# Performance work log

Hardware: AMD Instinct MI355X
Metric: run time of the kernel (lower is better)

Reference implementation:

```python
import jax, jax.numpy as jnp
import numpy as np

B, D, H = 524288, 64, 19  # batch, input_size, hidden_size


def setup_inputs() -> dict:
    key = jax.random.key(0)
    ks = jax.random.split(key, 4)
    x = jax.random.normal(ks[0], (B, D), dtype=jnp.float32)
    # nn.Linear params (stored as [out, in] like torch)
    Wi = jax.random.normal(ks[1], (H, D), dtype=jnp.float32) / np.sqrt(D).astype(np.float32)
    bi = jnp.zeros((H,), jnp.float32)
    Wr = jax.random.normal(ks[2], (H, H), dtype=jnp.float32) / np.sqrt(H).astype(np.float32)
    Wo = jax.random.normal(ks[3], (H, H), dtype=jnp.float32) / np.sqrt(H).astype(np.float32)
    bo = jnp.zeros((H,), jnp.float32)
    tau = jnp.full((H,), 0.5, jnp.float32)        # nn.Parameter(ones*0.5)
    tau_adapt = jnp.full((H,), 0.1, jnp.float32)  # nn.Parameter(ones*0.1)
    return {"x": x, "Wi": Wi, "bi": bi, "Wr": Wr, "Wo": Wo, "bo": bo,
            "tau": tau, "tau_adapt": tau_adapt, "steps": 10}


def reference(x, Wi, bi, Wr, Wo, bo, tau, tau_adapt, steps):
    dt = 0.01
    # scalar urgency over the whole input, clamped from below
    urgency = jnp.maximum(jnp.abs(x).mean(), 0.01)
    tau_dyn = jnp.clip(tau * (1.0 - tau_adapt) + tau_adapt / urgency, 0.01, 10.0)  # [H]
    mapped = x @ Wi.T + bi  # [B, H], computed once outside the loop
    h0 = jnp.zeros((x.shape[0], tau.shape[0]), x.dtype)

    def step(h, _):
        act = jnp.tanh(mapped + h @ Wr.T)
        h = h + dt * ((-h + act) / tau_dyn)
        return h, None

    h, _ = jax.lax.scan(step, h0, None, length=steps)
    return (h @ Wo.T + bo, h)
```

## Files before the change

kernel.cpp:

```cpp
#include <hip/hip_runtime.h>

#define NB 524288
#define ND 64
#define NH 19

__device__ __forceinline__ float fast_tanh(float x) {
    x = fminf(9.0f, fmaxf(-9.0f, x));
    float e = __expf(2.0f * x);
    return 1.0f - 2.0f * __builtin_amdgcn_rcpf(e + 1.0f);
}

extern "C" __global__ void __launch_bounds__(256)
ltc_mapped_urgency(const float* __restrict__ x, const float* __restrict__ Wi,
                   const float* __restrict__ bi, float* __restrict__ mapped,
                   double* __restrict__ acc, int storeMapped)
{
    const int b = blockIdx.x * 256 + threadIdx.x;
    const float4* xr = (const float4*)(x + (size_t)b * ND);
    float m[NH];
#pragma unroll
    for (int j = 0; j < NH; ++j) m[j] = bi[j];
    float s = 0.f;
#pragma unroll
    for (int q = 0; q < ND / 4; ++q) {
        const float4 v = xr[q];
        s += fabsf(v.x) + fabsf(v.y) + fabsf(v.z) + fabsf(v.w);
#pragma unroll
        for (int j = 0; j < NH; ++j) {
            m[j] = fmaf(v.x, Wi[j * ND + 4 * q + 0], m[j]);
            m[j] = fmaf(v.y, Wi[j * ND + 4 * q + 1], m[j]);
            m[j] = fmaf(v.z, Wi[j * ND + 4 * q + 2], m[j]);
            m[j] = fmaf(v.w, Wi[j * ND + 4 * q + 3], m[j]);
        }
    }
    if (storeMapped) {
#pragma unroll
        for (int j = 0; j < NH; ++j) mapped[(size_t)j * NB + b] = m[j];
    }
#pragma unroll
    for (int off = 32; off > 0; off >>= 1) s += __shfl_down(s, off, 64);
    __shared__ float red[4];
    const int lane = threadIdx.x & 63, w = threadIdx.x >> 6;
    if (lane == 0) red[w] = s;
    __syncthreads();
    if (threadIdx.x == 0) atomicAdd(acc, (double)(red[0] + red[1] + red[2] + red[3]));
}

template <bool RECOMP, int ROWS>
__global__ void __launch_bounds__(256)
ltc_steps(const float* __restrict__ x, const float* __restrict__ Wi,
          const float* __restrict__ bi, const float* __restrict__ mapped,
          const double* __restrict__ acc,
          const float* __restrict__ Wr, const float* __restrict__ Wo,
          const float* __restrict__ bo, const float* __restrict__ tau,
          const float* __restrict__ ta, const int* __restrict__ steps_p,
          float* __restrict__ out)
{
    const int gid = blockIdx.x * 256 + threadIdx.x;
    const int T = NB / ROWS;
    const double mean = *acc * (1.0 / ((double)NB * (double)ND));
    const float u = fmaxf((float)mean, 0.01f);
    float rr_[NH];
#pragma unroll
    for (int j = 0; j < NH; ++j) {
        float t = tau[j] * (1.f - ta[j]) + ta[j] / u;
        t = fminf(10.f, fmaxf(0.01f, t));
        rr_[j] = 0.01f / t;
    }
    float m[ROWS][NH], h[ROWS][NH];
#pragma unroll
    for (int rI = 0; rI < ROWS; ++rI) {
        const int b = gid + rI * T;
        if (RECOMP) {
            const float4* xr = (const float4*)(x + (size_t)b * ND);
#pragma unroll
            for (int j = 0; j < NH; ++j) m[rI][j] = bi[j];
#pragma unroll
            for (int q = 0; q < ND / 4; ++q) {
                const float4 v = xr[q];
#pragma unroll
                for (int j = 0; j < NH; ++j) {
                    m[rI][j] = fmaf(v.x, Wi[j * ND + 4 * q + 0], m[rI][j]);
                    m[rI][j] = fmaf(v.y, Wi[j * ND + 4 * q + 1], m[rI][j]);
                    m[rI][j] = fmaf(v.z, Wi[j * ND + 4 * q + 2], m[rI][j]);
                    m[rI][j] = fmaf(v.w, Wi[j * ND + 4 * q + 3], m[rI][j]);
                }
            }
        } else {
#pragma unroll
            for (int j = 0; j < NH; ++j) m[rI][j] = mapped[(size_t)j * NB + b];
        }
#pragma unroll
        for (int j = 0; j < NH; ++j) h[rI][j] = 0.f;
    }
    const int steps = *steps_p;
    for (int s = 0; s < steps; ++s) {
#pragma unroll
        for (int rI = 0; rI < ROWS; ++rI) {
            float a[NH];
#pragma unroll
            for (int j = 0; j < NH; ++j) {
                float p = m[rI][j];
#pragma unroll
                for (int k = 0; k < NH; ++k)
                    p = fmaf(h[rI][k], Wr[j * NH + k], p);
                a[j] = fast_tanh(p);
            }
#pragma unroll
            for (int j = 0; j < NH; ++j) h[rI][j] += rr_[j] * (a[j] - h[rI][j]);
        }
    }
#pragma unroll
    for (int rI = 0; rI < ROWS; ++rI) {
        const int b = gid + rI * T;
#pragma unroll
        for (int j = 0; j < NH; ++j) {
            float p = bo[j];
#pragma unroll
            for (int k = 0; k < NH; ++k) p = fmaf(h[rI][k], Wo[j * NH + k], p);
            out[(size_t)b * NH + j] = p;
        }
#pragma unroll
        for (int j = 0; j < NH; ++j)
            out[(size_t)NB * NH + (size_t)b * NH + j] = h[rI][j];
    }
}

extern "C" void kernel_launch(void* const* d_in, const int* in_sizes, int n_in,
                              void* d_out, int out_size, void* d_ws, size_t ws_size,
                              hipStream_t stream)
{
    const float* x   = (const float*)d_in[0];
    const float* Wi  = (const float*)d_in[1];
    const float* bi  = (const float*)d_in[2];
    const float* Wr  = (const float*)d_in[3];
    const float* Wo  = (const float*)d_in[4];
    const float* bo  = (const float*)d_in[5];
    const float* tau = (const float*)d_in[6];
    const float* ta  = (const float*)d_in[7];
    const int* steps = (const int*)d_in[8];
    float* out = (float*)d_out;

    double* acc = (double*)d_ws;
    float* mapped = (float*)((char*)d_ws + 16);
    const size_t need = 16 + (size_t)NB * NH * sizeof(float);
    const int storeMapped = (ws_size >= need) ? 1 : 0;

    hipMemsetAsync(d_ws, 0, sizeof(double), stream);
    ltc_mapped_urgency<<<NB / 256, 256, 0, stream>>>(x, Wi, bi, mapped, acc, storeMapped);

    constexpr int ROWS = 2;
    if (storeMapped)
        ltc_steps<false, ROWS><<<NB / ROWS / 256, 256, 0, stream>>>(
            x, Wi, bi, mapped, acc, Wr, Wo, bo, tau, ta, steps, out);
    else
        ltc_steps<true, ROWS><<<NB / ROWS / 256, 256, 0, stream>>>(
            x, Wi, bi, mapped, acc, Wr, Wo, bo, tau, ta, steps, out);
}
```

Measured before the change: 385.5 us.

## Stage output through shared memory for coalesced stores and rebalance rows per thread

The first kernel now processes two batch rows per thread, so each Wi weight load is reused across both rows. The step kernel drops to one row per thread and removes the recompute fallback. Its two outputs are staged in shared memory and written with coalesced float4 stores instead of strided per-thread scalar stores. This adds about 19 KB of LDS per block and extra barriers. It also assumes the workspace is always large enough to hold mapped.

```diff
diff --git a/kernel.cpp b/kernel.cpp
--- a/kernel.cpp
+++ b/kernel.cpp
@@ -10,33 +10,48 @@
     return 1.0f - 2.0f * __builtin_amdgcn_rcpf(e + 1.0f);
 }
 
+#define ROWS_A 2
 extern "C" __global__ void __launch_bounds__(256)
 ltc_mapped_urgency(const float* __restrict__ x, const float* __restrict__ Wi,
                    const float* __restrict__ bi, float* __restrict__ mapped,
-                   double* __restrict__ acc, int storeMapped)
+                   double* __restrict__ acc)
 {
-    const int b = blockIdx.x * 256 + threadIdx.x;
-    const float4* xr = (const float4*)(x + (size_t)b * ND);
-    float m[NH];
+    const int gid = blockIdx.x * 256 + threadIdx.x;
+    const int T = NB / ROWS_A;
+    float m[ROWS_A][NH];
 #pragma unroll
-    for (int j = 0; j < NH; ++j) m[j] = bi[j];
+    for (int r = 0; r < ROWS_A; ++r)
+#pragma unroll
+        for (int j = 0; j < NH; ++j) m[r][j] = bi[j];
     float s = 0.f;
 #pragma unroll
     for (int q = 0; q < ND / 4; ++q) {
-        const float4 v = xr[q];
-        s += fabsf(v.x) + fabsf(v.y) + fabsf(v.z) + fabsf(v.w);
+        float4 v[ROWS_A];
+#pragma unroll
+        for (int r = 0; r < ROWS_A; ++r) {
+            v[r] = ((const float4*)(x + (size_t)(gid + r * T) * ND))[q];
+            s += fabsf(v[r].x) + fabsf(v[r].y) + fabsf(v[r].z) + fabsf(v[r].w);
+        }
 #pragma unroll
         for (int j = 0; j < NH; ++j) {
-            m[j] = fmaf(v.x, Wi[j * ND + 4 * q + 0], m[j]);
-            m[j] = fmaf(v.y, Wi[j * ND + 4 * q + 1], m[j]);
-            m[j] = fmaf(v.z, Wi[j * ND + 4 * q + 2], m[j]);
-            m[j] = fmaf(v.w, Wi[j * ND + 4 * q + 3], m[j]);
+            const float w0 = Wi[j * ND + 4 * q + 0];
+            const float w1 = Wi[j * ND + 4 * q + 1];
+            const float w2 = Wi[j * ND + 4 * q + 2];
+            const float w3 = Wi[j * ND + 4 * q + 3];
+#pragma unroll
+            for (int r = 0; r < ROWS_A; ++r) {
+                m[r][j] = fmaf(v[r].x, w0, m[r][j]);
+                m[r][j] = fmaf(v[r].y, w1, m[r][j]);
+                m[r][j] = fmaf(v[r].z, w2, m[r][j]);
+                m[r][j] = fmaf(v[r].w, w3, m[r][j]);
+            }
         }
     }
-    if (storeMapped) {
 #pragma unroll
-        for (int j = 0; j < NH; ++j) mapped[(size_t)j * NB + b] = m[j];
-    }
+    for (int r = 0; r < ROWS_A; ++r)
+#pragma unroll
+        for (int j = 0; j < NH; ++j)
+            mapped[(size_t)j * NB + (gid + r * T)] = m[r][j];
 #pragma unroll
     for (int off = 32; off > 0; off >>= 1) s += __shfl_down(s, off, 64);
     __shared__ float red[4];
@@ -46,83 +61,72 @@
     if (threadIdx.x == 0) atomicAdd(acc, (double)(red[0] + red[1] + red[2] + red[3]));
 }
 
-template <bool RECOMP, int ROWS>
 __global__ void __launch_bounds__(256)
-ltc_steps(const float* __restrict__ x, const float* __restrict__ Wi,
-          const float* __restrict__ bi, const float* __restrict__ mapped,
-          const double* __restrict__ acc,
+ltc_steps(const float* __restrict__ mapped, const double* __restrict__ acc,
           const float* __restrict__ Wr, const float* __restrict__ Wo,
           const float* __restrict__ bo, const float* __restrict__ tau,
           const float* __restrict__ ta, const int* __restrict__ steps_p,
           float* __restrict__ out)
 {
-    const int gid = blockIdx.x * 256 + threadIdx.x;
-    const int T = NB / ROWS;
+    const int t = threadIdx.x;
+    const int b = blockIdx.x * 256 + t;
     const double mean = *acc * (1.0 / ((double)NB * (double)ND));
     const float u = fmaxf((float)mean, 0.01f);
-    float rr_[NH];
+    float rr[NH];
 #pragma unroll
     for (int j = 0; j < NH; ++j) {
-        float t = tau[j] * (1.f - ta[j]) + ta[j] / u;
-        t = fminf(10.f, fmaxf(0.01f, t));
-        rr_[j] = 0.01f / t;
+        float td = tau[j] * (1.f - ta[j]) + ta[j] / u;
+        td = fminf(10.f, fmaxf(0.01f, td));
+        rr[j] = 0.01f / td;
     }
-    float m[ROWS][NH], h[ROWS][NH];
+    float m[NH], h[NH];
 #pragma unroll
-    for (int rI = 0; rI < ROWS; ++rI) {
-        const int b = gid + rI * T;
-        if (RECOMP) {
-            const float4* xr = (const float4*)(x + (size_t)b * ND);
-#pragma unroll
-            for (int j = 0; j < NH; ++j) m[rI][j] = bi[j];
-#pragma unroll
-            for (int q = 0; q < ND / 4; ++q) {
-                const float4 v = xr[q];
-#pragma unroll
-                for (int j = 0; j < NH; ++j) {
-                    m[rI][j] = fmaf(v.x, Wi[j * ND + 4 * q + 0], m[rI][j]);
-                    m[rI][j] = fmaf(v.y, Wi[j * ND + 4 * q + 1], m[rI][j]);
-                    m[rI][j] = fmaf(v.z, Wi[j * ND + 4 * q + 2], m[rI][j]);
-                    m[rI][j] = fmaf(v.w, Wi[j * ND + 4 * q + 3], m[rI][j]);
-                }
-            }
-        } else {
-#pragma unroll
-            for (int j = 0; j < NH; ++j) m[rI][j] = mapped[(size_t)j * NB + b];
-        }
-#pragma unroll
-        for (int j = 0; j < NH; ++j) h[rI][j] = 0.f;
+    for (int j = 0; j < NH; ++j) {
+        m[j] = mapped[(size_t)j * NB + b];
+        h[j] = 0.f;
     }
     const int steps = *steps_p;
     for (int s = 0; s < steps; ++s) {
-#pragma unroll
-        for (int rI = 0; rI < ROWS; ++rI) {
-            float a[NH];
-#pragma unroll
-            for (int j = 0; j < NH; ++j) {
-                float p = m[rI][j];
-#pragma unroll
-                for (int k = 0; k < NH; ++k)
-                    p = fmaf(h[rI][k], Wr[j * NH + k], p);
-                a[j] = fast_tanh(p);
-            }
-#pragma unroll
-            for (int j = 0; j < NH; ++j) h[rI][j] += rr_[j] * (a[j] - h[rI][j]);
-        }
-    }
-#pragma unroll
-    for (int rI = 0; rI < ROWS; ++rI) {
-        const int b = gid + rI * T;
+        float a[NH];
 #pragma unroll
         for (int j = 0; j < NH; ++j) {
-            float p = bo[j];
+            float p = m[j];
 #pragma unroll
-            for (int k = 0; k < NH; ++k) p = fmaf(h[rI][k], Wo[j * NH + k], p);
-            out[(size_t)b * NH + j] = p;
+            for (int k = 0; k < NH; ++k)
+                p = fmaf(h[k], Wr[j * NH + k], p);
+            a[j] = fast_tanh(p);
         }
 #pragma unroll
-        for (int j = 0; j < NH; ++j)
-            out[(size_t)NB * NH + (size_t)b * NH + j] = h[rI][j];
+        for (int j = 0; j < NH; ++j) h[j] = fmaf(rr[j], a[j] - h[j], h[j]);
+    }
+    __shared__ float st[256 * NH];
+#pragma unroll
+    for (int j = 0; j < NH; ++j) {
+        float p = bo[j];
+#pragma unroll
+        for (int k = 0; k < NH; ++k) p = fmaf(h[k], Wo[j * NH + k], p);
+        st[t * NH + j] = p;
+    }
+    __syncthreads();
+    {
+        const float4* s4 = (const float4*)st;
+        float4* o4 = (float4*)(out + (size_t)blockIdx.x * 256 * NH);
+#pragma unroll
+        for (int i = 0; i < (256 * NH) / (4 * 256); ++i)
+            o4[t + i * 256] = s4[t + i * 256];
+        if (t + 1024 < 1216) o4[t + 1024] = s4[t + 1024];
+    }
+    __syncthreads();
+#pragma unroll
+    for (int j = 0; j < NH; ++j) st[t * NH + j] = h[j];
+    __syncthreads();
+    {
+        const float4* s4 = (const float4*)st;
+        float4* o4 = (float4*)(out + (size_t)NB * NH + (size_t)blockIdx.x * 256 * NH);
+#pragma unroll
+        for (int i = 0; i < (256 * NH) / (4 * 256); ++i)
+            o4[t + i * 256] = s4[t + i * 256];
+        if (t + 1024 < 1216) o4[t + 1024] = s4[t + 1024];
     }
 }
 
@@ -143,17 +147,8 @@
 
     double* acc = (double*)d_ws;
     float* mapped = (float*)((char*)d_ws + 16);
-    const size_t need = 16 + (size_t)NB * NH * sizeof(float);
-    const int storeMapped = (ws_size >= need) ? 1 : 0;
 
     hipMemsetAsync(d_ws, 0, sizeof(double), stream);
-    ltc_mapped_urgency<<<NB / 256, 256, 0, stream>>>(x, Wi, bi, mapped, acc, storeMapped);
-
-    constexpr int ROWS = 2;
-    if (storeMapped)
-        ltc_steps<false, ROWS><<<NB / ROWS / 256, 256, 0, stream>>>(
-            x, Wi, bi, mapped, acc, Wr, Wo, bo, tau, ta, steps, out);
-    else
-        ltc_steps<true, ROWS><<<NB / ROWS / 256, 256, 0, stream>>>(
-            x, Wi, bi, mapped, acc, Wr, Wo, bo, tau, ta, steps, out);
+    ltc_mapped_urgency<<<NB / ROWS_A / 256, 256, 0, stream>>>(x, Wi, bi, mapped, acc);
+    ltc_steps<<<NB / 256, 256, 0, stream>>>(mapped, acc, Wr, Wo, bo, tau, ta, steps, out);
 }
```

New measurement: 409.9 us. 1.06x slower.
